# Performance work log

Measured on AMD Instinct MI355X. Metric: run time of the kernel, lower is better.

The kernel has to match this reference:

```python
import jax, jax.numpy as jnp
import numpy as np

EMBED = 1024
HEADS = 16
HEAD_DIM = EMBED // HEADS


def setup_inputs() -> dict:
    key = jax.random.key(0)
    ks = jax.random.split(key, 8)
    N, S, E = 4, 2048, EMBED
    s = 1.0 / np.sqrt(E)
    return {
        "values": jax.random.normal(ks[0], (N, S, E), jnp.float32),
        "keys": jax.random.normal(ks[1], (N, S, E), jnp.float32),
        "queries": jax.random.normal(ks[2], (N, S, E), jnp.float32),
        # nn.Linear weights stored as (out_features, in_features)
        "Wv": jax.random.normal(ks[3], (E, E), jnp.float32) * s,
        "Wk": jax.random.normal(ks[4], (E, E), jnp.float32) * s,
        "Wq": jax.random.normal(ks[5], (E, E), jnp.float32) * s,
        "Wo": jax.random.normal(ks[6], (E, E), jnp.float32) * s,
        "bo": jax.random.normal(ks[7], (E,), jnp.float32) * s,
    }


def reference(values, keys, queries, Wv, Wk, Wq, Wo, bo):
    N = queries.shape[0]
    H, D, E = HEADS, HEAD_DIM, EMBED
    # projections (torch Linear: x @ W.T), reshape to [N, S, H, D]
    v = (values @ Wv.T).reshape(N, -1, H, D)
    k = (keys @ Wk.T).reshape(N, -1, H, D)
    q = (queries @ Wq.T).reshape(N, -1, H, D)
    energy = jnp.einsum("nqhd,nkhd->nhqk", q, k)
    # NOTE: original scales by sqrt(embed_size), not sqrt(head_dim)
    attn = jax.nn.softmax(energy / jnp.sqrt(jnp.float32(E)), axis=3)
    out = jnp.einsum("nhql,nlhd->nqhd", attn, v).reshape(N, -1, H * D)
    return out @ Wo.T + bo
```

## Files before the change

### kernel.cpp

```cpp
#include <hip/hip_runtime.h>

typedef __bf16  bf16x8 __attribute__((ext_vector_type(8)));
typedef float   f32x4  __attribute__((ext_vector_type(4)));
typedef unsigned short u16x8 __attribute__((ext_vector_type(8)));

__device__ __forceinline__ unsigned short f2bf(float f) {
    union { float f; unsigned int u; } v; v.f = f;
    unsigned int u = v.u;
    unsigned int r = (u + 0x7fffu + ((u >> 16) & 1u)) >> 16;
    return (unsigned short)r;
}

__device__ __forceinline__ unsigned int pkbf(float lo, float hi) {
    union { float f; unsigned int u; } a, b; a.f = lo; b.f = hi;
    return __builtin_amdgcn_perm(b.u + 0x8000u, a.u + 0x8000u, 0x07060302u);
}

__device__ __forceinline__ void gld_lds16(const unsigned short* g, unsigned short* l) {
    auto gp = (const __attribute__((address_space(1))) unsigned int*)(const void*)g;
    auto lp = (__attribute__((address_space(3))) unsigned int*)(unsigned int)(unsigned long long)(void*)l;
    __builtin_amdgcn_global_load_lds(gp, lp, 16, 0, 0);
}

__global__ void cast4_kernel(const float* __restrict__ a, const float* __restrict__ b,
                             const float* __restrict__ c, const float* __restrict__ d,
                             unsigned short* __restrict__ dst) {
    int sel = blockIdx.x >> 10;
    int off4 = (blockIdx.x & 1023) * 256 + threadIdx.x;
    const float* src = sel == 0 ? a : sel == 1 ? b : sel == 2 ? c : d;
    float4 f = ((const float4*)src)[off4];
    uint2 pk; pk.x = pkbf(f.x, f.y); pk.y = pkbf(f.z, f.w);
    ((uint2*)(dst + (size_t)sel * 1048576))[off4] = pk;
}

__global__ void cast_kernel(const float* __restrict__ src, unsigned short* __restrict__ dst, int n4) {
    int stride = gridDim.x * 256;
    for (int i = blockIdx.x * 256 + threadIdx.x; i < n4; i += stride) {
        float4 f = ((const float4*)src)[i];
        uint2 pk; pk.x = pkbf(f.x, f.y); pk.y = pkbf(f.z, f.w);
        ((uint2*)dst)[i] = pk;
    }
}

template <int MODE>
__global__ __launch_bounds__(256, 3)
void gemm_bt(const unsigned short* __restrict__ A, const unsigned short* __restrict__ Bt,
             void* __restrict__ dst, const float* __restrict__ bias, float a_scale)
{
    constexpr int K = 1024;
    __shared__ unsigned short As[128 * 32];
    __shared__ unsigned short Bs[128 * 32];

    const int t    = threadIdx.x;
    const int lane = t & 63;
    const int w    = t >> 6;
    const int q    = lane >> 4;
    const int ln   = lane & 15;
    const int wr   = w >> 1, wc = w & 1;
    const int m0   = blockIdx.y * 128;
    const int n0   = blockIdx.x * 128;

    f32x4 acc[4][4];
    const f32x4 zz = {0.f, 0.f, 0.f, 0.f};
#pragma unroll
    for (int i = 0; i < 4; ++i)
#pragma unroll
        for (int j = 0; j < 4; ++j) acc[i][j] = zz;

    const int srow = lane >> 2;
    const int scol = (lane & 3) * 8;

    for (int k0 = 0; k0 < K; k0 += 32) {
        __syncthreads();
#pragma unroll
        for (int c = 0; c < 2; ++c) {
            int u = w * 2 + c;
            gld_lds16(A  + (size_t)(m0 + u * 16 + srow) * K + k0 + scol, &As[u * 512]);
            gld_lds16(Bt + (size_t)(n0 + u * 16 + srow) * K + k0 + scol, &Bs[u * 512]);
        }
        __syncthreads();
        bf16x8 af[4], bf[4];
#pragma unroll
        for (int i = 0; i < 4; ++i)
            af[i] = *(const bf16x8*)&As[(wr * 64 + i * 16 + ln) * 32 + q * 8];
#pragma unroll
        for (int j = 0; j < 4; ++j)
            bf[j] = *(const bf16x8*)&Bs[(wc * 64 + j * 16 + ln) * 32 + q * 8];
#pragma unroll
        for (int i = 0; i < 4; ++i)
#pragma unroll
            for (int j = 0; j < 4; ++j)
                acc[i][j] = __builtin_amdgcn_mfma_f32_16x16x32_bf16(af[i], bf[j], acc[i][j], 0, 0, 0);
    }

#pragma unroll
    for (int i = 0; i < 4; ++i) {
#pragma unroll
        for (int j = 0; j < 4; ++j) {
            f32x4 c = acc[i][j];
            int mb = m0 + wr * 64 + i * 16 + q * 4;
            int nn = n0 + wc * 64 + j * 16 + ln;
            if constexpr (MODE == 1) {
                int b = mb >> 11, s = mb & 2047, h = nn >> 6, d = nn & 63;
                uint2 pk;
                pk.x = pkbf(c[0], c[1]);
                pk.y = pkbf(c[2], c[3]);
                size_t idx = (((size_t)(b * 16 + h) * 64) + d) * 2048 + s;
                *(uint2*)&((unsigned short*)dst)[idx] = pk;
            } else {
#pragma unroll
                for (int r = 0; r < 4; ++r) {
                    int m = mb + r;
                    float val = c[r] * a_scale;
                    if constexpr (MODE == 2) {
                        ((float*)dst)[(size_t)m * 1024 + nn] = val + bias[nn];
                    } else {
                        int b = m >> 11, s = m & 2047, h = nn >> 6, d = nn & 63;
                        size_t idx = (((size_t)(b * 16 + h) * 2048) + s) * 64 + d;
                        ((unsigned short*)dst)[idx] = f2bf(val);
                    }
                }
            }
        }
    }
}

__global__ __launch_bounds__(256, 3)
void attn_kernel(const unsigned short* __restrict__ Q, const unsigned short* __restrict__ Kg,
                 const unsigned short* __restrict__ Vt, unsigned short* __restrict__ Og)
{
    __shared__ unsigned short KP[128 * 136];
    __shared__ unsigned short Vs[4 * 2048];

    const int t    = threadIdx.x;
    const int lane = t & 63;
    const int w    = t >> 6;
    const int q    = lane >> 4;
    const int ln   = lane & 15;
    const int head = blockIdx.x;
    const int qt   = blockIdx.y;

    const unsigned short* Qh  = Q  + (size_t)head * 2048 * 64;
    const unsigned short* Kh  = Kg + (size_t)head * 2048 * 64;
    const unsigned short* Vth = Vt + (size_t)head * 64 * 2048;

    const int srow = lane >> 2;
    const int scol = (lane & 3) * 8;

    bf16x8 qf[2][2];
    const int rowb = qt * 128 + w * 32;
#pragma unroll
    for (int ti = 0; ti < 2; ++ti)
#pragma unroll
        for (int kc = 0; kc < 2; ++kc)
            qf[ti][kc] = *(const bf16x8*)&Qh[(size_t)(rowb + ti * 16 + ln) * 64 + kc * 32 + q * 8];

    const f32x4 zz = {0.f, 0.f, 0.f, 0.f};
    f32x4 oa[2][4];
#pragma unroll
    for (int ti = 0; ti < 2; ++ti)
#pragma unroll
        for (int dt = 0; dt < 4; ++dt) oa[ti][dt] = zz;
    float l_s[2] = {0.f, 0.f};

    for (int j = 0; j < 16; ++j) {
        __syncthreads();
#pragma unroll
        for (int c = 0; c < 4; ++c) {
            int u = w * 4 + c;
            int kc = u >> 3, rg = u & 7;
            gld_lds16(Kh + (size_t)(j * 128 + rg * 16 + srow) * 64 + kc * 32 + scol,
                      &KP[kc * 4096 + rg * 512]);
        }
#pragma unroll
        for (int c = 0; c < 4; ++c) {
            int u = w * 4 + c;
            int kv = u >> 2, rg = u & 3;
            gld_lds16(Vth + (size_t)(rg * 16 + srow) * 2048 + j * 128 + kv * 32 + scol,
                      &Vs[kv * 2048 + rg * 512]);
        }
        __syncthreads();

        f32x4 sa[8][2];
#pragma unroll
        for (int kt = 0; kt < 8; ++kt)
#pragma unroll
            for (int ti = 0; ti < 2; ++ti) sa[kt][ti] = zz;
#pragma unroll
        for (int kc = 0; kc < 2; ++kc) {
            bf16x8 ka[8];
#pragma unroll
            for (int kt = 0; kt < 8; ++kt)
                ka[kt] = *(const bf16x8*)&KP[kc * 4096 + (kt * 16 + ln) * 32 + q * 8];
#pragma unroll
            for (int kt = 0; kt < 8; ++kt)
#pragma unroll
                for (int ti = 0; ti < 2; ++ti)
                    sa[kt][ti] = __builtin_amdgcn_mfma_f32_16x16x32_bf16(ka[kt], qf[ti][kc], sa[kt][ti], 0, 0, 0);
        }
        __syncthreads();

#pragma unroll
        for (int ti = 0; ti < 2; ++ti) {
            float rs = 0.f;
            const int prow = w * 32 + ti * 16 + ln;
#pragma unroll
            for (int kt = 0; kt < 8; ++kt) {
                float p0 = exp2f(sa[kt][ti][0]);
                float p1 = exp2f(sa[kt][ti][1]);
                float p2 = exp2f(sa[kt][ti][2]);
                float p3 = exp2f(sa[kt][ti][3]);
                rs += (p0 + p1) + (p2 + p3);
                uint2 pk;
                pk.x = pkbf(p0, p1);
                pk.y = pkbf(p2, p3);
                *(uint2*)&KP[prow * 136 + kt * 16 + q * 4] = pk;
            }
            rs += __shfl_xor(rs, 16);
            rs += __shfl_xor(rs, 32);
            l_s[ti] += rs;
        }

#pragma unroll
        for (int kc = 0; kc < 4; ++kc) {
            bf16x8 va[4], pb[2];
#pragma unroll
            for (int dt = 0; dt < 4; ++dt)
                va[dt] = *(const bf16x8*)&Vs[kc * 2048 + (dt * 16 + ln) * 32 + q * 8];
#pragma unroll
            for (int ti = 0; ti < 2; ++ti)
                pb[ti] = *(const bf16x8*)&KP[(w * 32 + ti * 16 + ln) * 136 + kc * 32 + q * 8];
#pragma unroll
            for (int ti = 0; ti < 2; ++ti)
#pragma unroll
                for (int dt = 0; dt < 4; ++dt)
                    oa[ti][dt] = __builtin_amdgcn_mfma_f32_16x16x32_bf16(va[dt], pb[ti], oa[ti][dt], 0, 0, 0);
        }
    }

    const int n = head >> 4;
    const int hbase = (head & 15) * 64;
#pragma unroll
    for (int ti = 0; ti < 2; ++ti) {
        float inv = 1.f / l_s[ti];
        int sr = qt * 128 + w * 32 + ti * 16 + ln;
        size_t base = ((size_t)n * 2048 + sr) * 1024 + hbase;
#pragma unroll
        for (int dt = 0; dt < 4; ++dt) {
            uint2 pk;
            pk.x = pkbf(oa[ti][dt][0] * inv, oa[ti][dt][1] * inv);
            pk.y = pkbf(oa[ti][dt][2] * inv, oa[ti][dt][3] * inv);
            *(uint2*)&Og[base + dt * 16 + q * 4] = pk;
        }
    }
}

extern "C" void kernel_launch(void* const* d_in, const int* in_sizes, int n_in,
                              void* d_out, int out_size, void* d_ws, size_t ws_size,
                              hipStream_t stream)
{
    (void)in_sizes; (void)n_in; (void)out_size; (void)ws_size;
    const float* values  = (const float*)d_in[0];
    const float* keys    = (const float*)d_in[1];
    const float* queries = (const float*)d_in[2];
    const float* Wv = (const float*)d_in[3];
    const float* Wk = (const float*)d_in[4];
    const float* Wq = (const float*)d_in[5];
    const float* Wo = (const float*)d_in[6];
    const float* bo = (const float*)d_in[7];
    float* out = (float*)d_out;

    unsigned short* ws   = (unsigned short*)d_ws;
    unsigned short* Wv_b = ws;
    unsigned short* Wk_b = ws + 1048576;
    unsigned short* Wq_b = ws + 2097152;
    unsigned short* Wo_b = ws + 3145728;
    unsigned short* Act  = ws + 4194304;
    unsigned short* Ob   = Act;
    unsigned short* Qb   = ws + 12582912;
    unsigned short* Kb   = Qb + 8388608;
    unsigned short* Vtb  = Kb + 8388608;

    cast4_kernel<<<4096, 256, 0, stream>>>(Wv, Wk, Wq, Wo, ws);

    dim3 g(8, 64), b(256);
    const float qscale = 1.4426950408889634f / 32.f;

    cast_kernel<<<4096, 256, 0, stream>>>(values, Act, 2097152);
    gemm_bt<1><<<g, b, 0, stream>>>(Act, Wv_b, Vtb, nullptr, 1.f);
    cast_kernel<<<4096, 256, 0, stream>>>(keys, Act, 2097152);
    gemm_bt<0><<<g, b, 0, stream>>>(Act, Wk_b, Kb, nullptr, 1.f);
    cast_kernel<<<4096, 256, 0, stream>>>(queries, Act, 2097152);
    gemm_bt<0><<<g, b, 0, stream>>>(Act, Wq_b, Qb, nullptr, qscale);

    attn_kernel<<<dim3(64, 16), b, 0, stream>>>(Qb, Kb, Vtb, Ob);
    gemm_bt<2><<<g, b, 0, stream>>>(Ob, Wo_b, out, bo, 1.f);
}
```

Measured before the change: 405.3 us.

## Double-buffer LDS tiles in GEMM and attention with one barrier per step

Both the projection GEMM and the attention kernel now prefetch the next K/V or A/B tile into a second LDS buffer while computing on the current one, using a single barrier per iteration. Attention switches to 64-key tiles with a separate per-warp P buffer, which removes the barrier between score computation and PV accumulation. The GEMM grid is also transposed so adjacent blocks walk along M, changing L2 reuse of the weight tiles. The cost is more LDS per block in the GEMM, and twice as many loop iterations of smaller work in attention.

```diff
diff --git a/kernel.cpp b/kernel.cpp
--- a/kernel.cpp
+++ b/kernel.cpp
@@ -48,8 +48,8 @@
              void* __restrict__ dst, const float* __restrict__ bias, float a_scale)
 {
     constexpr int K = 1024;
-    __shared__ unsigned short As[128 * 32];
-    __shared__ unsigned short Bs[128 * 32];
+    __shared__ unsigned short As[2][4096];
+    __shared__ unsigned short Bs[2][4096];
 
     const int t    = threadIdx.x;
     const int lane = t & 63;
@@ -57,8 +57,10 @@
     const int q    = lane >> 4;
     const int ln   = lane & 15;
     const int wr   = w >> 1, wc = w & 1;
-    const int m0   = blockIdx.y * 128;
-    const int n0   = blockIdx.x * 128;
+    const int m0   = blockIdx.x * 128;
+    const int n0   = blockIdx.y * 128;
+    const int srow = lane >> 2;
+    const int scol = (lane & 3) * 8;
 
     f32x4 acc[4][4];
     const f32x4 zz = {0.f, 0.f, 0.f, 0.f};
@@ -67,30 +69,32 @@
 #pragma unroll
         for (int j = 0; j < 4; ++j) acc[i][j] = zz;
 
-    const int srow = lane >> 2;
-    const int scol = (lane & 3) * 8;
-
-    for (int k0 = 0; k0 < K; k0 += 32) {
-        __syncthreads();
+    auto stage = [&](int k0, int p) {
 #pragma unroll
         for (int c = 0; c < 2; ++c) {
             int u = w * 2 + c;
-            gld_lds16(A  + (size_t)(m0 + u * 16 + srow) * K + k0 + scol, &As[u * 512]);
-            gld_lds16(Bt + (size_t)(n0 + u * 16 + srow) * K + k0 + scol, &Bs[u * 512]);
-        }
+            gld_lds16(A  + (size_t)(m0 + u * 16 + srow) * K + k0 + scol, &As[p][u * 512]);
+            gld_lds16(Bt + (size_t)(n0 + u * 16 + srow) * K + k0 + scol, &Bs[p][u * 512]);
+        }
+    };
+
+    stage(0, 0);
+    for (int j = 0; j < 32; ++j) {
         __syncthreads();
-        bf16x8 af[4], bf[4];
+        if (j < 31) stage((j + 1) * 32, (j + 1) & 1);
+        const int p = j & 1;
+        bf16x8 af[4], bfr[4];
 #pragma unroll
         for (int i = 0; i < 4; ++i)
-            af[i] = *(const bf16x8*)&As[(wr * 64 + i * 16 + ln) * 32 + q * 8];
-#pragma unroll
-        for (int j = 0; j < 4; ++j)
-            bf[j] = *(const bf16x8*)&Bs[(wc * 64 + j * 16 + ln) * 32 + q * 8];
+            af[i] = *(const bf16x8*)&As[p][(wr * 64 + i * 16 + ln) * 32 + q * 8];
+#pragma unroll
+        for (int jj = 0; jj < 4; ++jj)
+            bfr[jj] = *(const bf16x8*)&Bs[p][(wc * 64 + jj * 16 + ln) * 32 + q * 8];
 #pragma unroll
         for (int i = 0; i < 4; ++i)
 #pragma unroll
-            for (int j = 0; j < 4; ++j)
-                acc[i][j] = __builtin_amdgcn_mfma_f32_16x16x32_bf16(af[i], bf[j], acc[i][j], 0, 0, 0);
+            for (int jj = 0; jj < 4; ++jj)
+                acc[i][jj] = __builtin_amdgcn_mfma_f32_16x16x32_bf16(af[i], bfr[jj], acc[i][jj], 0, 0, 0);
     }
 
 #pragma unroll
@@ -129,8 +133,9 @@
 void attn_kernel(const unsigned short* __restrict__ Q, const unsigned short* __restrict__ Kg,
                  const unsigned short* __restrict__ Vt, unsigned short* __restrict__ Og)
 {
-    __shared__ unsigned short KP[128 * 136];
-    __shared__ unsigned short Vs[4 * 2048];
+    __shared__ unsigned short Ks[2][4096];
+    __shared__ unsigned short Vs[2][4096];
+    __shared__ unsigned short Ps[128 * 72];
 
     const int t    = threadIdx.x;
     const int lane = t & 63;
@@ -163,49 +168,48 @@
         for (int dt = 0; dt < 4; ++dt) oa[ti][dt] = zz;
     float l_s[2] = {0.f, 0.f};
 
-    for (int j = 0; j < 16; ++j) {
+    auto stage = [&](int j, int p) {
+#pragma unroll
+        for (int c = 0; c < 2; ++c) {
+            int u = w * 2 + c;
+            int kc = u >> 2, rg = u & 3;
+            gld_lds16(Kh + (size_t)(j * 64 + rg * 16 + srow) * 64 + kc * 32 + scol,
+                      &Ks[p][kc * 2048 + rg * 512]);
+            gld_lds16(Vth + (size_t)(rg * 16 + srow) * 2048 + j * 64 + kc * 32 + scol,
+                      &Vs[p][kc * 2048 + rg * 512]);
+        }
+    };
+
+    stage(0, 0);
+    for (int j = 0; j < 32; ++j) {
         __syncthreads();
-#pragma unroll
-        for (int c = 0; c < 4; ++c) {
-            int u = w * 4 + c;
-            int kc = u >> 3, rg = u & 7;
-            gld_lds16(Kh + (size_t)(j * 128 + rg * 16 + srow) * 64 + kc * 32 + scol,
-                      &KP[kc * 4096 + rg * 512]);
-        }
-#pragma unroll
-        for (int c = 0; c < 4; ++c) {
-            int u = w * 4 + c;
-            int kv = u >> 2, rg = u & 3;
-            gld_lds16(Vth + (size_t)(rg * 16 + srow) * 2048 + j * 128 + kv * 32 + scol,
-                      &Vs[kv * 2048 + rg * 512]);
-        }
-        __syncthreads();
-
-        f32x4 sa[8][2];
-#pragma unroll
-        for (int kt = 0; kt < 8; ++kt)
+        if (j < 31) stage(j + 1, (j + 1) & 1);
+        const int p = j & 1;
+
+        f32x4 sa[4][2];
+#pragma unroll
+        for (int kt = 0; kt < 4; ++kt)
 #pragma unroll
             for (int ti = 0; ti < 2; ++ti) sa[kt][ti] = zz;
 #pragma unroll
         for (int kc = 0; kc < 2; ++kc) {
-            bf16x8 ka[8];
-#pragma unroll
-            for (int kt = 0; kt < 8; ++kt)
-                ka[kt] = *(const bf16x8*)&KP[kc * 4096 + (kt * 16 + ln) * 32 + q * 8];
-#pragma unroll
-            for (int kt = 0; kt < 8; ++kt)
+            bf16x8 ka[4];
+#pragma unroll
+            for (int kt = 0; kt < 4; ++kt)
+                ka[kt] = *(const bf16x8*)&Ks[p][kc * 2048 + (kt * 16 + ln) * 32 + q * 8];
+#pragma unroll
+            for (int kt = 0; kt < 4; ++kt)
 #pragma unroll
                 for (int ti = 0; ti < 2; ++ti)
                     sa[kt][ti] = __builtin_amdgcn_mfma_f32_16x16x32_bf16(ka[kt], qf[ti][kc], sa[kt][ti], 0, 0, 0);
         }
-        __syncthreads();
 
 #pragma unroll
         for (int ti = 0; ti < 2; ++ti) {
             float rs = 0.f;
             const int prow = w * 32 + ti * 16 + ln;
 #pragma unroll
-            for (int kt = 0; kt < 8; ++kt) {
+            for (int kt = 0; kt < 4; ++kt) {
                 float p0 = exp2f(sa[kt][ti][0]);
                 float p1 = exp2f(sa[kt][ti][1]);
                 float p2 = exp2f(sa[kt][ti][2]);
@@ -214,7 +218,7 @@
                 uint2 pk;
                 pk.x = pkbf(p0, p1);
                 pk.y = pkbf(p2, p3);
-                *(uint2*)&KP[prow * 136 + kt * 16 + q * 4] = pk;
+                *(uint2*)&Ps[prow * 72 + kt * 16 + q * 4] = pk;
             }
             rs += __shfl_xor(rs, 16);
             rs += __shfl_xor(rs, 32);
@@ -222,14 +226,14 @@
         }
 
 #pragma unroll
-        for (int kc = 0; kc < 4; ++kc) {
+        for (int kc = 0; kc < 2; ++kc) {
             bf16x8 va[4], pb[2];
 #pragma unroll
             for (int dt = 0; dt < 4; ++dt)
-                va[dt] = *(const bf16x8*)&Vs[kc * 2048 + (dt * 16 + ln) * 32 + q * 8];
+                va[dt] = *(const bf16x8*)&Vs[p][kc * 2048 + (dt * 16 + ln) * 32 + q * 8];
 #pragma unroll
             for (int ti = 0; ti < 2; ++ti)
-                pb[ti] = *(const bf16x8*)&KP[(w * 32 + ti * 16 + ln) * 136 + kc * 32 + q * 8];
+                pb[ti] = *(const bf16x8*)&Ps[(w * 32 + ti * 16 + ln) * 72 + kc * 32 + q * 8];
 #pragma unroll
             for (int ti = 0; ti < 2; ++ti)
 #pragma unroll
@@ -283,7 +287,7 @@
 
     cast4_kernel<<<4096, 256, 0, stream>>>(Wv, Wk, Wq, Wo, ws);
 
-    dim3 g(8, 64), b(256);
+    dim3 g(64, 8), b(256);
     const float qscale = 1.4426950408889634f / 32.f;
 
     cast_kernel<<<4096, 256, 0, stream>>>(values, Act, 2097152);
```

After: 373.7 us. -7.8%, faster.
